# Kernel optimization log

Measured on AMD Instinct MI355X. Metric: run time of the kernel, lower is better.

## Reference

```python
import jax, jax.numpy as jnp
import numpy as np

N_NODES = 100000
N_EDGES = 1600000
N_GRAPHS = 2048
F_IN = 33
D = 256


def _graph_conv(x, edge_index, w_rel, b_rel, w_root):
    # PyG GraphConv (aggr='add'): out = lin_rel(sum_j x_j) + lin_root(x)
    src, dst = edge_index[0], edge_index[1]
    agg = jax.ops.segment_sum(x[src], dst, num_segments=x.shape[0])  # [N, F]
    return agg @ w_rel + b_rel + x @ w_root


def setup_inputs() -> dict:
    key = jax.random.key(0)
    ks = jax.random.split(key, 16)
    scale_in = 1.0 / np.sqrt(F_IN)
    scale_d = 1.0 / np.sqrt(D)
    inp = {
        "x": jax.random.normal(ks[0], (N_NODES, F_IN), dtype=jnp.float32),
        "edge_index": jax.random.randint(ks[1], (2, N_EDGES), 0, N_NODES),
        "batch_index": jnp.sort(jax.random.randint(ks[2], (N_NODES,), 0, N_GRAPHS)),
        # initial_conv: GraphConv(F_IN -> D)
        "w_rel0": jax.random.normal(ks[3], (F_IN, D), dtype=jnp.float32) * scale_in,
        "b_rel0": jnp.zeros((D,), dtype=jnp.float32),
        "w_root0": jax.random.normal(ks[4], (F_IN, D), dtype=jnp.float32) * scale_in,
        # conv1..conv3: GraphConv(D -> D)
        "w_rel1": jax.random.normal(ks[5], (D, D), dtype=jnp.float32) * scale_d,
        "b_rel1": jnp.zeros((D,), dtype=jnp.float32),
        "w_root1": jax.random.normal(ks[6], (D, D), dtype=jnp.float32) * scale_d,
        "w_rel2": jax.random.normal(ks[7], (D, D), dtype=jnp.float32) * scale_d,
        "b_rel2": jnp.zeros((D,), dtype=jnp.float32),
        "w_root2": jax.random.normal(ks[8], (D, D), dtype=jnp.float32) * scale_d,
        "w_rel3": jax.random.normal(ks[9], (D, D), dtype=jnp.float32) * scale_d,
        "b_rel3": jnp.zeros((D,), dtype=jnp.float32),
        "w_root3": jax.random.normal(ks[10], (D, D), dtype=jnp.float32) * scale_d,
        # output head Linear(D -> 1)
        "w_out": jax.random.normal(ks[11], (D, 1), dtype=jnp.float32) * scale_d,
        "b_out": jnp.zeros((1,), dtype=jnp.float32),
    }
    return inp


def reference(x, edge_index, batch_index,
              w_rel0, b_rel0, w_root0,
              w_rel1, b_rel1, w_root1,
              w_rel2, b_rel2, w_root2,
              w_rel3, b_rel3, w_root3,
              w_out, b_out):
    # dropout omitted (eval mode)
    h = jax.nn.gelu(_graph_conv(x, edge_index, w_rel0, b_rel0, w_root0))
    h = jax.nn.gelu(_graph_conv(h, edge_index, w_rel1, b_rel1, w_root1))
    h = jax.nn.gelu(_graph_conv(h, edge_index, w_rel2, b_rel2, w_root2))
    h = jax.nn.gelu(_graph_conv(h, edge_index, w_rel3, b_rel3, w_root3))
    # global mean pool over graphs
    sums = jax.ops.segment_sum(h, batch_index, num_segments=N_GRAPHS)          # [G, D]
    counts = jax.ops.segment_sum(jnp.ones((h.shape[0],), h.dtype), batch_index,
                                 num_segments=N_GRAPHS)                         # [G]
    pooled = sums / jnp.maximum(counts, 1.0)[:, None]
    return pooled @ w_out + b_out                                               # [G, 1]
```

## Files before the change

### kernel.cpp

```cpp
#include <hip/hip_runtime.h>
#include <math.h>

#define NN 100000
#define NE 1600000
#define NG 2048
#define FIN 33
#define DD 256

#define SH 8
#define NB ((NN + 255) >> 8)
#define CH 4096
#define PCAP 4608
#define ESCAP 6144

#define RBLKS ((NN + 255) / 256)

typedef __attribute__((ext_vector_type(8))) short bf16x8;
typedef __attribute__((ext_vector_type(4))) float f32x4;

__device__ __forceinline__ float b2f(unsigned short u){
    union { unsigned int i; float f; } c; c.i = ((unsigned int)u) << 16; return c.f;
}
__device__ __forceinline__ unsigned short f2b(float f){
    union { float f; unsigned int u; } c; c.f = f;
    unsigned int r = c.u + 0x7fffu + ((c.u >> 16) & 1u);
    return (unsigned short)(r >> 16);
}

__device__ __forceinline__ float gelu_tanh(float x){
    float x3 = x * x * x;
    float t = tanhf(0.7978845608028654f * (x + 0.044715f * x3));
    return 0.5f * x * (1.0f + t);
}

__global__ __launch_bounds__(256) void k_bin(const int* __restrict__ src,
                                             const int* __restrict__ dst,
                                             int* __restrict__ gcur,
                                             int2* __restrict__ pairs){
    __shared__ int cnt[NB];
    __shared__ int lb[NB];
    __shared__ int gbase[NB];
    __shared__ int sc[512];
    __shared__ int2 stage[CH];

    int t = threadIdx.x;
    for(int i = t; i < NB; i += 256) cnt[i] = 0;
    __syncthreads();

    int e0 = blockIdx.x * CH;
    int n = NE - e0; if(n > CH) n = CH;

    int  myb[16];
    int  myr[16];
    int2 myp[16];
    #pragma unroll
    for(int k = 0; k < 16; k++){
        int e = e0 + t + k * 256;
        if(e < NE){
            int s = src[e], d = dst[e];
            int b = d >> SH;
            myr[k] = atomicAdd(&cnt[b], 1);
            myb[k] = b;
            myp[k] = make_int2(s, d);
        } else myb[k] = -1;
    }
    __syncthreads();

    sc[t]       = (t       < NB) ? cnt[t]       : 0;
    sc[t + 256] = (t + 256 < NB) ? cnt[t + 256] : 0;
    __syncthreads();
    for(int off = 1; off < 512; off <<= 1){
        int a  = (t >= off)       ? sc[t - off]       : 0;
        int b2 = (t + 256 >= off) ? sc[t + 256 - off] : 0;
        __syncthreads();
        sc[t] += a; sc[t + 256] += b2;
        __syncthreads();
    }
    for(int i = t; i < NB; i += 256){
        lb[i] = sc[i] - cnt[i];
        int c = cnt[i];
        gbase[i] = (c > 0) ? atomicAdd(&gcur[i], c) : 0;
    }
    __syncthreads();

    #pragma unroll
    for(int k = 0; k < 16; k++){
        if(myb[k] >= 0) stage[lb[myb[k]] + myr[k]] = myp[k];
    }
    __syncthreads();

    for(int i = t; i < n; i += 256){
        int2 p = stage[i];
        int b = p.y >> SH;
        int tgt = gbase[b] + (i - lb[b]);
        if(tgt < PCAP) pairs[(size_t)b * PCAP + tgt] = p;
    }
}

__global__ void k_sscan(const int* __restrict__ gcur, int* __restrict__ boff){
    __shared__ int s[512];
    int t = threadIdx.x;
    int v = 0;
    if(t < NB){ v = gcur[t]; if(v > PCAP) v = PCAP; }
    s[t] = v; __syncthreads();
    for(int off = 1; off < 512; off <<= 1){
        int u = (t >= off) ? s[t - off] : 0;
        __syncthreads();
        s[t] += u;
        __syncthreads();
    }
    if(t < NB) boff[t] = s[t] - v;
}

__global__ __launch_bounds__(256) void k_bcsr(const int2* __restrict__ pairs,
                                              const int* __restrict__ gcur,
                                              const int* __restrict__ boff,
                                              int* __restrict__ deg,
                                              int* __restrict__ rs,
                                              int* __restrict__ esrc){
    __shared__ int hist[256];
    __shared__ int sc[256];
    __shared__ int cur2[256];
    __shared__ int est[ESCAP];

    int b = blockIdx.x;
    int t = threadIdx.x;
    int m = gcur[b]; if(m > PCAP) m = PCAP;
    int pstart = boff[b];
    const int2* bp = pairs + (size_t)b * PCAP;

    hist[t] = 0;
    __syncthreads();
    for(int i = t; i < m; i += 256) atomicAdd(&hist[bp[i].y & 255], 1);
    __syncthreads();

    sc[t] = hist[t]; __syncthreads();
    for(int off = 1; off < 256; off <<= 1){
        int u = (t >= off) ? sc[t - off] : 0;
        __syncthreads();
        sc[t] += u;
        __syncthreads();
    }
    int excl = sc[t] - hist[t];
    cur2[t] = excl;
    int node = (b << 8) + t;
    if(node < NN){
        deg[node] = hist[t];
        rs[node]  = pstart + excl;
    }
    __syncthreads();

    for(int i = t; i < m; i += 256){
        int2 p = bp[i];
        int pos = atomicAdd(&cur2[p.y & 255], 1);
        if(pos < ESCAP) est[pos] = p.x;
        else esrc[pstart + pos] = p.x;
    }
    __syncthreads();
    int lim = (m < ESCAP) ? m : ESCAP;
    for(int i = t; i < lim; i += 256) esrc[pstart + i] = est[i];
}

__global__ void k_xpad(const float* __restrict__ x, unsigned short* __restrict__ xb){
    int idx = blockIdx.x * 256 + threadIdx.x;
    if(idx >= NN * 64) return;
    int n = idx >> 6, c = idx & 63;
    xb[idx] = (c < FIN) ? f2b(x[(size_t)n * FIN + c]) : 0;
}

__global__ void k_aggx(const unsigned short* __restrict__ xb, const int* __restrict__ rs,
                       const int* __restrict__ deg, const int* __restrict__ esrc,
                       unsigned short* __restrict__ axb){
    int wv = (blockIdx.x * blockDim.x + threadIdx.x) >> 6;
    int lane = threadIdx.x & 63;
    int node = wv * 4 + (lane >> 4);
    int l16 = lane & 15;
    if(node >= NN) return;
    int start = rs[node], cnt = deg[node];
    float a0 = 0.f, a1 = 0.f, a2 = 0.f, a3 = 0.f;
    const unsigned short* xp = xb + l16 * 4;
    int j = 0;
    for(; j + 4 <= cnt; j += 4){
        int e0 = esrc[start+j], e1 = esrc[start+j+1], e2 = esrc[start+j+2], e3 = esrc[start+j+3];
        ushort4 v0 = *(const ushort4*)(xp + (size_t)e0 * 64);
        ushort4 v1 = *(const ushort4*)(xp + (size_t)e1 * 64);
        ushort4 v2 = *(const ushort4*)(xp + (size_t)e2 * 64);
        ushort4 v3 = *(const ushort4*)(xp + (size_t)e3 * 64);
        a0 += (b2f(v0.x) + b2f(v1.x)) + (b2f(v2.x) + b2f(v3.x));
        a1 += (b2f(v0.y) + b2f(v1.y)) + (b2f(v2.y) + b2f(v3.y));
        a2 += (b2f(v0.z) + b2f(v1.z)) + (b2f(v2.z) + b2f(v3.z));
        a3 += (b2f(v0.w) + b2f(v1.w)) + (b2f(v2.w) + b2f(v3.w));
    }
    for(; j < cnt; j++){
        int e = esrc[start + j];
        ushort4 v = *(const ushort4*)(xp + (size_t)e * 64);
        a0 += b2f(v.x); a1 += b2f(v.y); a2 += b2f(v.z); a3 += b2f(v.w);
    }
    ushort4 o; o.x = f2b(a0); o.y = f2b(a1); o.z = f2b(a2); o.w = f2b(a3);
    *(ushort4*)(axb + (size_t)node * 64 + l16 * 4) = o;
}

__global__ void k_agg256(const unsigned short* __restrict__ h, const int* __restrict__ rs,
                         const int* __restrict__ deg, const int* __restrict__ esrc,
                         unsigned short* __restrict__ agg){
    int wv = (blockIdx.x * blockDim.x + threadIdx.x) >> 6;
    int lane = threadIdx.x & 63;
    int node = wv * 2 + (lane >> 5);
    int l32 = lane & 31;
    if(node >= NN) return;
    int start = rs[node], cnt = deg[node];
    float a[8] = {0.f,0.f,0.f,0.f,0.f,0.f,0.f,0.f};
    const unsigned short* hp = h + l32 * 8;
    int j = 0;
    for(; j + 8 <= cnt; j += 8){
        bf16x8 v[8];
        #pragma unroll
        for(int q = 0; q < 8; q++){
            int e = esrc[start + j + q];
            v[q] = *(const bf16x8*)(hp + (size_t)e * DD);
        }
        #pragma unroll
        for(int q = 0; q < 8; q++)
            #pragma unroll
            for(int d = 0; d < 8; d++)
                a[d] += b2f((unsigned short)v[q][d]);
    }
    for(; j < cnt; j++){
        int e = esrc[start + j];
        bf16x8 v = *(const bf16x8*)(hp + (size_t)e * DD);
        #pragma unroll
        for(int d = 0; d < 8; d++) a[d] += b2f((unsigned short)v[d]);
    }
    bf16x8 o;
    #pragma unroll
    for(int d = 0; d < 8; d++) o[d] = (short)f2b(a[d]);
    *(bf16x8*)(agg + (size_t)node * DD + l32 * 8) = o;
}

__global__ void k_wt(const float* __restrict__ W, unsigned short* __restrict__ Bt){
    __shared__ float s[16][17];
    int tx = threadIdx.x, ty = threadIdx.y;
    int k = blockIdx.y * 16 + ty;
    int j = blockIdx.x * 16 + tx;
    s[ty][tx] = W[k * DD + j];
    __syncthreads();
    Bt[(size_t)(blockIdx.x * 16 + ty) * DD + blockIdx.y * 16 + tx] = f2b(s[tx][ty]);
}

__global__ void k_wt0(const float* __restrict__ W, unsigned short* __restrict__ Bt){
    int idx = blockIdx.x * 256 + threadIdx.x;
    if(idx >= DD * 64) return;
    int j = idx >> 6, k = idx & 63;
    Bt[idx] = (k < FIN) ? f2b(W[(size_t)k * DD + j]) : 0;
}

template<int KS, int AST>
__global__ __launch_bounds__(512, 4) void k_mfma_gemm(
    const unsigned short* __restrict__ A0, const unsigned short* __restrict__ A1,
    const unsigned short* __restrict__ Bt0, const unsigned short* __restrict__ Bt1,
    const float* __restrict__ bias, unsigned short* __restrict__ out)
{
    constexpr int KHALF = KS * 32;
    constexpr int KTOT  = 2 * KHALF;
    constexpr int BST   = KTOT + 8;
    __shared__ unsigned short Bs[64 * BST];

    int t = threadIdx.x;
    int lane = t & 63;
    int w = t >> 6;
    int r16 = lane & 15;
    int kg  = lane >> 4;

    int bid = blockIdx.x;
    int rblk = (bid >> 5) * 8 + (bid & 7);
    int j0p  = (bid >> 3) & 3;
    if(rblk >= RBLKS) return;
    int i0 = rblk * 256;
    int jbase = j0p * 64;

    constexpr int SEG = KTOT / 8;
    #pragma unroll
    for(int p = 0; p < (64 * SEG) / 512; p++){
        int idx = p * 512 + t;
        int row = idx / SEG;
        int k = (idx % SEG) * 8;
        bf16x8 v;
        if(k < KHALF) v = *(const bf16x8*)(Bt0 + (size_t)(jbase + row) * AST + k);
        else          v = *(const bf16x8*)(Bt1 + (size_t)(jbase + row) * AST + (k - KHALF));
        *(bf16x8*)(&Bs[row * BST + k]) = v;
    }
    __syncthreads();

    int baseRow = i0 + w * 32;
    auto loadA = [&](int ks, bf16x8* af){
        const unsigned short* Ap = (ks < KS) ? A0 : A1;
        int kk = ((ks < KS) ? ks : ks - KS) * 32 + kg * 8;
        #pragma unroll
        for(int m = 0; m < 2; m++){
            int gi = baseRow + m * 16 + r16;
            if(gi > NN - 1) gi = NN - 1;
            af[m] = *(const bf16x8*)(Ap + (size_t)gi * AST + kk);
        }
    };

    f32x4 acc[2][4];
    #pragma unroll
    for(int m = 0; m < 2; m++)
        #pragma unroll
        for(int n = 0; n < 4; n++)
            acc[m][n] = (f32x4){0.f, 0.f, 0.f, 0.f};

    bf16x8 afb[2][2];
    loadA(0, afb[0]);
    loadA(1, afb[1]);

    #pragma unroll
    for(int ks = 0; ks < 2 * KS; ks++){
        bf16x8 bfr[4];
        #pragma unroll
        for(int n = 0; n < 4; n++)
            bfr[n] = *(const bf16x8*)(&Bs[(n * 16 + r16) * BST + ks * 32 + kg * 8]);
        #pragma unroll
        for(int m = 0; m < 2; m++)
            #pragma unroll
            for(int n = 0; n < 4; n++)
                acc[m][n] = __builtin_amdgcn_mfma_f32_16x16x32_bf16(afb[ks & 1][m], bfr[n], acc[m][n], 0, 0, 0);
        if(ks + 2 < 2 * KS) loadA(ks + 2, afb[ks & 1]);
    }

    int rg = kg * 4;
    #pragma unroll
    for(int n = 0; n < 4; n++){
        int gj = jbase + n * 16 + r16;
        float bb = bias[gj];
        #pragma unroll
        for(int m = 0; m < 2; m++){
            #pragma unroll
            for(int r = 0; r < 4; r++){
                int gi = baseRow + m * 16 + rg + r;
                if(gi < NN)
                    out[(size_t)gi * DD + gj] = f2b(gelu_tanh(acc[m][n][r] + bb));
            }
        }
    }
}

__global__ void k_pool(const unsigned short* __restrict__ h, const int* __restrict__ batch,
                       const float* __restrict__ wout, float* __restrict__ gsum,
                       int* __restrict__ gcnt){
    int w = (blockIdx.x * blockDim.x + threadIdx.x) >> 6;
    int lane = threadIdx.x & 63;
    if(w >= NN) return;
    ushort4 hv = *(const ushort4*)(h + (size_t)w * DD + lane * 4);
    float4 wv = *(const float4*)(wout + lane * 4);
    float d = b2f(hv.x)*wv.x + b2f(hv.y)*wv.y + b2f(hv.z)*wv.z + b2f(hv.w)*wv.w;
    for(int off = 32; off > 0; off >>= 1) d += __shfl_down(d, off);
    if(lane == 0){
        int g = batch[w];
        atomicAdd(&gsum[g], d);
        atomicAdd(&gcnt[g], 1);
    }
}

__global__ void k_final(const float* __restrict__ gsum, const int* __restrict__ gcnt,
                        const float* __restrict__ bout, float* __restrict__ out){
    int g = blockIdx.x * 256 + threadIdx.x;
    if(g < NG) out[g] = gsum[g] / fmaxf((float)gcnt[g], 1.f) + bout[0];
}

extern "C" void kernel_launch(void* const* d_in, const int* in_sizes, int n_in,
                              void* d_out, int out_size, void* d_ws, size_t ws_size,
                              hipStream_t stream){
    const float* x       = (const float*)d_in[0];
    const int*   ei      = (const int*)d_in[1];
    const int*   src     = ei;
    const int*   dst     = ei + NE;
    const int*   batch   = (const int*)d_in[2];
    const float* w_rel0  = (const float*)d_in[3];
    const float* b_rel0  = (const float*)d_in[4];
    const float* w_root0 = (const float*)d_in[5];
    const float* w_rel1  = (const float*)d_in[6];
    const float* b_rel1  = (const float*)d_in[7];
    const float* w_root1 = (const float*)d_in[8];
    const float* w_rel2  = (const float*)d_in[9];
    const float* b_rel2  = (const float*)d_in[10];
    const float* w_root2 = (const float*)d_in[11];
    const float* w_rel3  = (const float*)d_in[12];
    const float* b_rel3  = (const float*)d_in[13];
    const float* w_root3 = (const float*)d_in[14];
    const float* w_out   = (const float*)d_in[15];
    const float* b_out   = (const float*)d_in[16];
    float* out = (float*)d_out;

    char* ws = (char*)d_ws;
    size_t off = 0;
    auto alloc = [&](size_t bytes) -> void* {
        void* p = ws + off;
        off = (off + bytes + 255) & ~(size_t)255;
        return p;
    };
    unsigned short* hA  = (unsigned short*)alloc((size_t)NN * DD * 2);
    unsigned short* hB  = (unsigned short*)alloc((size_t)NN * DD * 2);
    unsigned short* agg = (unsigned short*)alloc((size_t)NN * DD * 2);
    int*   deg  = (int*)alloc((size_t)NN * 4);
    int*   rs   = (int*)alloc((size_t)NN * 4);
    int*   esrc = (int*)alloc((size_t)NE * 4);
    int*   gcur = (int*)alloc(512 * 4);
    int*   boff = (int*)alloc(512 * 4);
    float* gsum = (float*)alloc((size_t)NG * 4);
    int*   gcnt = (int*)alloc((size_t)NG * 4);
    unsigned short* bt[6];
    for(int i = 0; i < 6; i++) bt[i] = (unsigned short*)alloc((size_t)DD * DD * 2);
    unsigned short* bt0r = (unsigned short*)alloc((size_t)DD * 64 * 2);
    unsigned short* bt0o = (unsigned short*)alloc((size_t)DD * 64 * 2);
    (void)ws_size; (void)in_sizes; (void)n_in; (void)out_size;

    int2* pairs = (int2*)hB;
    unsigned short* xb  = agg;
    unsigned short* axb = agg + (size_t)NN * 64 + 128;

    hipMemsetAsync(gcur, 0, 512 * 4, stream);
    k_bin<<<(NE + CH - 1) / CH, 256, 0, stream>>>(src, dst, gcur, pairs);
    k_sscan<<<1, 512, 0, stream>>>(gcur, boff);
    k_bcsr<<<NB, 256, 0, stream>>>(pairs, gcur, boff, deg, rs, esrc);

    dim3 wtg(16, 16), wtb(16, 16);
    k_wt<<<wtg, wtb, 0, stream>>>(w_rel1,  bt[0]);
    k_wt<<<wtg, wtb, 0, stream>>>(w_root1, bt[1]);
    k_wt<<<wtg, wtb, 0, stream>>>(w_rel2,  bt[2]);
    k_wt<<<wtg, wtb, 0, stream>>>(w_root2, bt[3]);
    k_wt<<<wtg, wtb, 0, stream>>>(w_rel3,  bt[4]);
    k_wt<<<wtg, wtb, 0, stream>>>(w_root3, bt[5]);
    k_wt0<<<(DD * 64 + 255) / 256, 256, 0, stream>>>(w_rel0,  bt0r);
    k_wt0<<<(DD * 64 + 255) / 256, 256, 0, stream>>>(w_root0, bt0o);
    k_xpad<<<(NN * 64 + 255) / 256, 256, 0, stream>>>(x, xb);

    int aggGrid  = (NN + 3) / 4;
    int agg2Grid = (NN * 32 + 255) / 256;
    int gemmGrid = ((RBLKS + 7) / 8) * 32;

    k_aggx<<<(NN + 15) / 16, 256, 0, stream>>>(xb, rs, deg, esrc, axb);
    k_mfma_gemm<2, 64><<<gemmGrid, 512, 0, stream>>>(axb, xb, bt0r, bt0o, b_rel0, hA);
    k_agg256<<<agg2Grid, 256, 0, stream>>>(hA, rs, deg, esrc, agg);
    k_mfma_gemm<8, 256><<<gemmGrid, 512, 0, stream>>>(agg, hA, bt[0], bt[1], b_rel1, hB);
    k_agg256<<<agg2Grid, 256, 0, stream>>>(hB, rs, deg, esrc, agg);
    k_mfma_gemm<8, 256><<<gemmGrid, 512, 0, stream>>>(agg, hB, bt[2], bt[3], b_rel2, hA);
    k_agg256<<<agg2Grid, 256, 0, stream>>>(hA, rs, deg, esrc, agg);
    k_mfma_gemm<8, 256><<<gemmGrid, 512, 0, stream>>>(agg, hA, bt[4], bt[5], b_rel3, hB);

    hipMemsetAsync(gsum, 0, (size_t)NG * 4, stream);
    hipMemsetAsync(gcnt, 0, (size_t)NG * 4, stream);
    k_pool<<<aggGrid, 256, 0, stream>>>(hB, batch, w_out, gsum, gcnt);
    k_final<<<(NG + 255) / 256, 256, 0, stream>>>(gsum, gcnt, b_out, out);
}
```

Measured before the change: 821.8 us.

## Widen GEMM column tile to 128 and batch weight-transpose launches

The MFMA GEMM block now covers 128 output columns instead of 64, halving the grid so each A row tile is read from global memory twice instead of four times. The B tile is staged in two phases (rel then root weights) through a shared-memory buffer sized for one half of K, with an extra barrier between phases. Accumulators double to 2x8 per wave, which raises register pressure and may lower occupancy under the 512x4 launch bounds. The six weight-transpose launches are merged into one 3D-grid launch, the two layer-0 transposes into one, and the two pool memsets into one, cutting launch overhead.

```diff
diff --git a/kernel.cpp b/kernel.cpp
--- a/kernel.cpp
+++ b/kernel.cpp
@@ -237,8 +237,12 @@
     *(bf16x8*)(agg + (size_t)node * DD + l32 * 8) = o;
 }
 
-__global__ void k_wt(const float* __restrict__ W, unsigned short* __restrict__ Bt){
+struct WPtrs { const float* w[6]; };
+
+__global__ void k_wt6(WPtrs wp, unsigned short* __restrict__ btAll){
     __shared__ float s[16][17];
+    const float* W = wp.w[blockIdx.z];
+    unsigned short* Bt = btAll + (size_t)blockIdx.z * DD * DD;
     int tx = threadIdx.x, ty = threadIdx.y;
     int k = blockIdx.y * 16 + ty;
     int j = blockIdx.x * 16 + tx;
@@ -247,9 +251,13 @@
     Bt[(size_t)(blockIdx.x * 16 + ty) * DD + blockIdx.y * 16 + tx] = f2b(s[tx][ty]);
 }
 
-__global__ void k_wt0(const float* __restrict__ W, unsigned short* __restrict__ Bt){
+struct W2Ptrs { const float* w[2]; };
+
+__global__ void k_wt0(W2Ptrs wp, unsigned short* __restrict__ btAll){
     int idx = blockIdx.x * 256 + threadIdx.x;
     if(idx >= DD * 64) return;
+    const float* W = wp.w[blockIdx.z];
+    unsigned short* Bt = btAll + (size_t)blockIdx.z * DD * 64;
     int j = idx >> 6, k = idx & 63;
     Bt[idx] = (k < FIN) ? f2b(W[(size_t)k * DD + j]) : 0;
 }
@@ -260,10 +268,10 @@
     const unsigned short* __restrict__ Bt0, const unsigned short* __restrict__ Bt1,
     const float* __restrict__ bias, unsigned short* __restrict__ out)
 {
-    constexpr int KHALF = KS * 32;
-    constexpr int KTOT  = 2 * KHALF;
-    constexpr int BST   = KTOT + 8;
-    __shared__ unsigned short Bs[64 * BST];
+    constexpr int CK  = KS * 32;
+    constexpr int BST = CK + 8;
+    constexpr int SEG = CK / 8;
+    __shared__ unsigned short Bs[128 * BST];
 
     int t = threadIdx.x;
     int lane = t & 63;
@@ -272,29 +280,23 @@
     int kg  = lane >> 4;
 
     int bid = blockIdx.x;
-    int rblk = (bid >> 5) * 8 + (bid & 7);
-    int j0p  = (bid >> 3) & 3;
+    int rblk = (bid >> 4) * 8 + (bid & 7);
+    int chalf = (bid >> 3) & 1;
     if(rblk >= RBLKS) return;
     int i0 = rblk * 256;
-    int jbase = j0p * 64;
-
-    constexpr int SEG = KTOT / 8;
-    #pragma unroll
-    for(int p = 0; p < (64 * SEG) / 512; p++){
-        int idx = p * 512 + t;
-        int row = idx / SEG;
-        int k = (idx % SEG) * 8;
-        bf16x8 v;
-        if(k < KHALF) v = *(const bf16x8*)(Bt0 + (size_t)(jbase + row) * AST + k);
-        else          v = *(const bf16x8*)(Bt1 + (size_t)(jbase + row) * AST + (k - KHALF));
-        *(bf16x8*)(&Bs[row * BST + k]) = v;
-    }
-    __syncthreads();
-
+    int jbase = chalf * 128;
     int baseRow = i0 + w * 32;
-    auto loadA = [&](int ks, bf16x8* af){
-        const unsigned short* Ap = (ks < KS) ? A0 : A1;
-        int kk = ((ks < KS) ? ks : ks - KS) * 32 + kg * 8;
+
+    f32x4 acc[2][8];
+    #pragma unroll
+    for(int m = 0; m < 2; m++)
+        #pragma unroll
+        for(int n = 0; n < 8; n++)
+            acc[m][n] = (f32x4){0.f, 0.f, 0.f, 0.f};
+
+    auto loadA = [&](int gks, bf16x8* af){
+        const unsigned short* Ap = (gks < KS) ? A0 : A1;
+        int kk = ((gks < KS) ? gks : gks - KS) * 32 + kg * 8;
         #pragma unroll
         for(int m = 0; m < 2; m++){
             int gi = baseRow + m * 16 + r16;
@@ -303,34 +305,39 @@
         }
     };
 
-    f32x4 acc[2][4];
-    #pragma unroll
-    for(int m = 0; m < 2; m++)
-        #pragma unroll
-        for(int n = 0; n < 4; n++)
-            acc[m][n] = (f32x4){0.f, 0.f, 0.f, 0.f};
-
     bf16x8 afb[2][2];
     loadA(0, afb[0]);
     loadA(1, afb[1]);
 
     #pragma unroll
-    for(int ks = 0; ks < 2 * KS; ks++){
-        bf16x8 bfr[4];
-        #pragma unroll
-        for(int n = 0; n < 4; n++)
-            bfr[n] = *(const bf16x8*)(&Bs[(n * 16 + r16) * BST + ks * 32 + kg * 8]);
-        #pragma unroll
-        for(int m = 0; m < 2; m++)
+    for(int c = 0; c < 2; c++){
+        const unsigned short* Bp = c ? Bt1 : Bt0;
+        if(c) __syncthreads();
+        #pragma unroll
+        for(int p = 0; p < (128 * SEG) / 512; p++){
+            int idx = p * 512 + t;
+            int row = idx / SEG;
+            int k8 = (idx % SEG) * 8;
+            *(bf16x8*)(&Bs[row * BST + k8]) =
+                *(const bf16x8*)(Bp + (size_t)(jbase + row) * AST + k8);
+        }
+        __syncthreads();
+        #pragma unroll
+        for(int ksl = 0; ksl < KS; ksl++){
+            int gks = c * KS + ksl;
             #pragma unroll
-            for(int n = 0; n < 4; n++)
-                acc[m][n] = __builtin_amdgcn_mfma_f32_16x16x32_bf16(afb[ks & 1][m], bfr[n], acc[m][n], 0, 0, 0);
-        if(ks + 2 < 2 * KS) loadA(ks + 2, afb[ks & 1]);
+            for(int n = 0; n < 8; n++){
+                bf16x8 bfr = *(const bf16x8*)(&Bs[(n * 16 + r16) * BST + ksl * 32 + kg * 8]);
+                acc[0][n] = __builtin_amdgcn_mfma_f32_16x16x32_bf16(afb[gks & 1][0], bfr, acc[0][n], 0, 0, 0);
+                acc[1][n] = __builtin_amdgcn_mfma_f32_16x16x32_bf16(afb[gks & 1][1], bfr, acc[1][n], 0, 0, 0);
+            }
+            if(gks + 2 < 2 * KS) loadA(gks + 2, afb[gks & 1]);
+        }
     }
 
     int rg = kg * 4;
     #pragma unroll
-    for(int n = 0; n < 4; n++){
+    for(int n = 0; n < 8; n++){
         int gj = jbase + n * 16 + r16;
         float bb = bias[gj];
         #pragma unroll
@@ -409,10 +416,8 @@
     int*   boff = (int*)alloc(512 * 4);
     float* gsum = (float*)alloc((size_t)NG * 4);
     int*   gcnt = (int*)alloc((size_t)NG * 4);
-    unsigned short* bt[6];
-    for(int i = 0; i < 6; i++) bt[i] = (unsigned short*)alloc((size_t)DD * DD * 2);
-    unsigned short* bt0r = (unsigned short*)alloc((size_t)DD * 64 * 2);
-    unsigned short* bt0o = (unsigned short*)alloc((size_t)DD * 64 * 2);
+    unsigned short* btAll = (unsigned short*)alloc((size_t)6 * DD * DD * 2);
+    unsigned short* bt0All = (unsigned short*)alloc((size_t)2 * DD * 64 * 2);
     (void)ws_size; (void)in_sizes; (void)n_in; (void)out_size;
 
     int2* pairs = (int2*)hB;
@@ -424,20 +429,21 @@
     k_sscan<<<1, 512, 0, stream>>>(gcur, boff);
     k_bcsr<<<NB, 256, 0, stream>>>(pairs, gcur, boff, deg, rs, esrc);
 
-    dim3 wtg(16, 16), wtb(16, 16);
-    k_wt<<<wtg, wtb, 0, stream>>>(w_rel1,  bt[0]);
-    k_wt<<<wtg, wtb, 0, stream>>>(w_root1, bt[1]);
-    k_wt<<<wtg, wtb, 0, stream>>>(w_rel2,  bt[2]);
-    k_wt<<<wtg, wtb, 0, stream>>>(w_root2, bt[3]);
-    k_wt<<<wtg, wtb, 0, stream>>>(w_rel3,  bt[4]);
-    k_wt<<<wtg, wtb, 0, stream>>>(w_root3, bt[5]);
-    k_wt0<<<(DD * 64 + 255) / 256, 256, 0, stream>>>(w_rel0,  bt0r);
-    k_wt0<<<(DD * 64 + 255) / 256, 256, 0, stream>>>(w_root0, bt0o);
+    WPtrs wp; wp.w[0] = w_rel1; wp.w[1] = w_root1; wp.w[2] = w_rel2;
+    wp.w[3] = w_root2; wp.w[4] = w_rel3; wp.w[5] = w_root3;
+    k_wt6<<<dim3(16, 16, 6), dim3(16, 16), 0, stream>>>(wp, btAll);
+    W2Ptrs w2; w2.w[0] = w_rel0; w2.w[1] = w_root0;
+    k_wt0<<<dim3((DD * 64 + 255) / 256, 1, 2), 256, 0, stream>>>(w2, bt0All);
     k_xpad<<<(NN * 64 + 255) / 256, 256, 0, stream>>>(x, xb);
+
+    unsigned short* bt[6];
+    for(int i = 0; i < 6; i++) bt[i] = btAll + (size_t)i * DD * DD;
+    unsigned short* bt0r = bt0All;
+    unsigned short* bt0o = bt0All + (size_t)DD * 64;
 
     int aggGrid  = (NN + 3) / 4;
     int agg2Grid = (NN * 32 + 255) / 256;
-    int gemmGrid = ((RBLKS + 7) / 8) * 32;
+    int gemmGrid = ((RBLKS + 7) / 8) * 16;
 
     k_aggx<<<(NN + 15) / 16, 256, 0, stream>>>(xb, rs, deg, esrc, axb);
     k_mfma_gemm<2, 64><<<gemmGrid, 512, 0, stream>>>(axb, xb, bt0r, bt0o, b_rel0, hA);
@@ -448,8 +454,8 @@
     k_agg256<<<agg2Grid, 256, 0, stream>>>(hA, rs, deg, esrc, agg);
     k_mfma_gemm<8, 256><<<gemmGrid, 512, 0, stream>>>(agg, hA, bt[4], bt[5], b_rel3, hB);
 
-    hipMemsetAsync(gsum, 0, (size_t)NG * 4, stream);
-    hipMemsetAsync(gcnt, 0, (size_t)NG * 4, stream);
+    size_t poolBytes = (size_t)((char*)(gcnt + NG) - (char*)gsum);
+    hipMemsetAsync(gsum, 0, poolBytes, stream);
     k_pool<<<aggGrid, 256, 0, stream>>>(hB, batch, w_out, gsum, gcnt);
     k_final<<<(NG + 255) / 256, 256, 0, stream>>>(gsum, gcnt, b_out, out);
 }
```

After: 785.9 us. -4.4%, faster.
